# Kernel tuning notes

Measured on AMD Instinct MI355X. Metric: run time of the kernel, lower is better.

The kernel has to match this reference:

```python
import jax, jax.numpy as jnp
import numpy as np

B, S, H = 4, 1024, 1024
NH = 16
DH = H // NH  # 64


def setup_inputs() -> dict:
    key = jax.random.key(0)
    ks = jax.random.split(key, 8)
    std = 1.0 / np.sqrt(H)
    return {
        "query": jax.random.normal(ks[0], (B, S, H), jnp.float32),
        "key": jax.random.normal(ks[1], (B, S, H), jnp.float32),
        "value": jax.random.normal(ks[2], (B, S, H), jnp.float32),
        "masks": jnp.ones((B, S), jnp.float32),
        "Wq": jax.random.normal(ks[3], (H, H), jnp.float32) * std,
        "bq": jnp.zeros((H,), jnp.float32),
        "Wk": jax.random.normal(ks[4], (H, H), jnp.float32) * std,
        "bk": jnp.zeros((H,), jnp.float32),
        "Wv": jax.random.normal(ks[5], (H, H), jnp.float32) * std,
        "bv": jnp.zeros((H,), jnp.float32),
    }


def reference(query, key, value, masks, Wq, bq, Wk, bk, Wv, bv):
    # ReLU-gated projections (torch Linear: x @ W.T + b)
    qp = jax.nn.relu(jnp.einsum("bsh,oh->bso", query, Wq) + bq)
    kp = jax.nn.relu(jnp.einsum("bsh,oh->bso", key, Wk) + bk)
    vp = jax.nn.relu(jnp.einsum("bsh,oh->bso", value, Wv) + bv)
    # chunk(dim=2)+cat(dim=0) == split hidden into (NH, DH) contiguous slices
    qh = qp.reshape(B, S, NH, DH)
    kh = kp.reshape(B, S, NH, DH)
    vh = vp.reshape(B, S, NH, DH)
    scale = 1.0 / jnp.sqrt(jnp.asarray(DH, qp.dtype))
    # [B, NH, Sq, Sk]
    alpha = jnp.einsum("bqnd,bknd->bnqk", qh, kh) * scale
    alpha = jax.nn.softmax(alpha, axis=-1)
    # post-softmax multiplicative mask, applied per QUERY position
    alpha = alpha * masks[:, None, :, None]
    hiddens = jnp.einsum("bnqk,bknd->bqnd", alpha, vh).reshape(B, S, H)
    return hiddens + query
```

## Files before the change

kernel.cpp:

```cpp
#include <hip/hip_runtime.h>


typedef __attribute__((ext_vector_type(8))) __bf16 bf16x8;
typedef __attribute__((ext_vector_type(4))) float f32x4;
typedef __attribute__((ext_vector_type(16))) float f32x16;
typedef __attribute__((ext_vector_type(8))) unsigned short u16x8;
typedef __attribute__((ext_vector_type(4))) unsigned short u16x4;

#define XQ_OFF 0u
#define XK_OFF 4194304u
#define XV_OFF 8388608u
#define WQ_OFF 12582912u
#define WK_OFF 13631488u
#define WV_OFF 14680064u
#define QP_OFF 15728640u
#define KP_OFF 19922944u
#define VT_OFF 24117248u

__device__ __forceinline__ unsigned short f2bf(float f) {
  union { float f; unsigned int u; } c; c.f = f;
  return (unsigned short)((c.u + 0x7fffu + ((c.u >> 16) & 1u)) >> 16);
}

__global__ __launch_bounds__(256) void cvt_kernel(
    const float* __restrict__ q, const float* __restrict__ k, const float* __restrict__ v,
    const float* __restrict__ wq, const float* __restrict__ wk, const float* __restrict__ wv,
    unsigned short* __restrict__ ws) {
  const int z = blockIdx.y;
  const float* src; unsigned short* dst; int n;
  switch (z) {
    case 0: src = q;  dst = ws + XQ_OFF; n = 4194304; break;
    case 1: src = k;  dst = ws + XK_OFF; n = 4194304; break;
    case 2: src = v;  dst = ws + XV_OFF; n = 4194304; break;
    case 3: src = wq; dst = ws + WQ_OFF; n = 1048576; break;
    case 4: src = wk; dst = ws + WK_OFF; n = 1048576; break;
    default: src = wv; dst = ws + WV_OFF; n = 1048576; break;
  }
  const int i8 = (blockIdx.x * 256 + threadIdx.x) * 8;
  if (i8 >= n) return;
  const float4 f0 = *(const float4*)(src + i8);
  const float4 f1 = *(const float4*)(src + i8 + 4);
  u16x8 r;
  r[0] = f2bf(f0.x); r[1] = f2bf(f0.y); r[2] = f2bf(f0.z); r[3] = f2bf(f0.w);
  r[4] = f2bf(f1.x); r[5] = f2bf(f1.y); r[6] = f2bf(f1.z); r[7] = f2bf(f1.w);
  *(u16x8*)(dst + i8) = r;
}

__global__ __launch_bounds__(256) void proj_gemm(
    unsigned short* __restrict__ ws,
    const float* __restrict__ bq, const float* __restrict__ bk, const float* __restrict__ bv) {
  __shared__ unsigned short smem[24576];
  const int z = blockIdx.z;
  const unsigned short* X = ws + (z == 0 ? XQ_OFF : z == 1 ? XK_OFF : XV_OFF);
  const unsigned short* W = ws + (z == 0 ? WQ_OFF : z == 1 ? WK_OFF : WV_OFF);
  unsigned short* P = ws + (z == 0 ? QP_OFF : z == 1 ? KP_OFF : VT_OFF);
  const float* bias = z == 0 ? bq : z == 1 ? bk : bv;

  const int tid  = threadIdx.x;
  const int lane = tid & 63;
  const int w    = tid >> 6;
  const int l31  = lane & 31;
  const int g    = lane >> 5;
  const int wr = w >> 1, wc = w & 1;

  const int lin = blockIdx.x + 8 * blockIdx.y;
  const int xcd = lin & 7;
  const int idx = lin >> 3;
  const int m0 = (xcd * 4 + (idx >> 3)) * 128;
  const int n0 = (idx & 7) * 128;

  f32x16 acc[2][2];
#pragma unroll
  for (int i = 0; i < 2; ++i)
#pragma unroll
    for (int j = 0; j < 2; ++j)
#pragma unroll
      for (int r = 0; r < 16; ++r) acc[i][j][r] = 0.f;

  const int c1 = 256 + tid;
  const int row0 = tid >> 2, kc0 = (((tid & 3) ^ ((row0 >> 1) & 3)) * 8);
  const int row1 = c1 >> 2,  kc1 = (((c1 & 3) ^ ((row1 >> 1) & 3)) * 8);
  const unsigned short* gA0 = X + (size_t)(m0 + row0) * 1024 + kc0;
  const unsigned short* gA1 = X + (size_t)(m0 + row1) * 1024 + kc1;
  const unsigned short* gB0 = W + (size_t)(n0 + row0) * 1024 + kc0;
  const unsigned short* gB1 = W + (size_t)(n0 + row1) * 1024 + kc1;
  const int d0 = w * 512, d1 = 2048 + w * 512;

  auto stage = [&](int buf) {
    unsigned short* Ab = smem + buf * 8192;
    unsigned short* Bb = Ab + 4096;
    __builtin_amdgcn_global_load_lds((const __attribute__((address_space(1))) void*)gA0,
                                     (__attribute__((address_space(3))) void*)(Ab + d0), 16, 0, 0);
    __builtin_amdgcn_global_load_lds((const __attribute__((address_space(1))) void*)gB0,
                                     (__attribute__((address_space(3))) void*)(Bb + d0), 16, 0, 0);
    __builtin_amdgcn_global_load_lds((const __attribute__((address_space(1))) void*)gA1,
                                     (__attribute__((address_space(3))) void*)(Ab + d1), 16, 0, 0);
    __builtin_amdgcn_global_load_lds((const __attribute__((address_space(1))) void*)gB1,
                                     (__attribute__((address_space(3))) void*)(Bb + d1), 16, 0, 0);
    gA0 += 32; gA1 += 32; gB0 += 32; gB1 += 32;
  };
  auto compute = [&](int buf) {
    const unsigned short* Ab = smem + buf * 8192;
    const unsigned short* Bb = Ab + 4096;
    bf16x8 af[2][2], bfv[2][2];
#pragma unroll
    for (int mt = 0; mt < 2; ++mt)
#pragma unroll
      for (int kk = 0; kk < 2; ++kk) {
        const int ra = wr * 64 + mt * 32 + l31;
        af[mt][kk] = *(const bf16x8*)&Ab[ra * 32 + (((kk * 2 + g) ^ ((ra >> 1) & 3)) * 8)];
      }
#pragma unroll
    for (int nt = 0; nt < 2; ++nt)
#pragma unroll
      for (int kk = 0; kk < 2; ++kk) {
        const int rb = wc * 64 + nt * 32 + l31;
        bfv[nt][kk] = *(const bf16x8*)&Bb[rb * 32 + (((kk * 2 + g) ^ ((rb >> 1) & 3)) * 8)];
      }
#pragma unroll
    for (int mt = 0; mt < 2; ++mt)
#pragma unroll
      for (int nt = 0; nt < 2; ++nt)
#pragma unroll
        for (int kk = 0; kk < 2; ++kk)
          acc[mt][nt] = __builtin_amdgcn_mfma_f32_32x32x16_bf16(af[mt][kk], bfv[nt][kk],
                                                                acc[mt][nt], 0, 0, 0);
  };

  stage(0); stage(1);
  for (int t = 0; t < 31; ++t) {
    asm volatile("s_waitcnt vmcnt(4)" ::: "memory");
    __builtin_amdgcn_s_barrier();
    if (t < 30) stage((t + 2) % 3);
    compute(t % 3);
  }
  asm volatile("s_waitcnt vmcnt(0)" ::: "memory");
  __builtin_amdgcn_s_barrier();
  compute(31 % 3);

  asm volatile("s_waitcnt lgkmcnt(0)" ::: "memory");
  __builtin_amdgcn_s_barrier();

  unsigned short* Tw = smem + w * 4608;
  if (z != 2) {
#pragma unroll
    for (int mt = 0; mt < 2; ++mt)
#pragma unroll
      for (int nt = 0; nt < 2; ++nt) {
        const float bvv = bias[n0 + wc * 64 + nt * 32 + l31];
#pragma unroll
        for (int reg = 0; reg < 16; ++reg) {
          const int rloc = (reg & 3) + 8 * (reg >> 2) + 4 * g;
          float v = acc[mt][nt][reg] + bvv;
          v = v > 0.f ? v : 0.f;
          Tw[(mt * 32 + rloc) * 72 + nt * 32 + l31] = f2bf(v);
        }
      }
    const int row0g = m0 + wr * 64;
    const int colb  = n0 + wc * 64;
#pragma unroll
    for (int i = 0; i < 8; ++i) {
      const int rr = i * 8 + (lane >> 3);
      const int cc = (lane & 7) * 8;
      *(u16x8*)&P[(size_t)(row0g + rr) * 1024 + colb + cc] = *(const u16x8*)&Tw[rr * 72 + cc];
    }
  } else {
#pragma unroll
    for (int mt = 0; mt < 2; ++mt)
#pragma unroll
      for (int nt = 0; nt < 2; ++nt) {
        const float bvv = bias[n0 + wc * 64 + nt * 32 + l31];
#pragma unroll
        for (int rq = 0; rq < 4; ++rq) {
          u16x4 pk;
#pragma unroll
          for (int r = 0; r < 4; ++r) {
            float v = acc[mt][nt][rq * 4 + r] + bvv;
            v = v > 0.f ? v : 0.f;
            pk[r] = f2bf(v);
          }
          *(u16x4*)&Tw[(nt * 32 + l31) * 72 + mt * 32 + rq * 8 + g * 4] = pk;
        }
      }
    const int h2 = (n0 >> 6) + wc;
    const int bb = m0 >> 10;
    const int s0 = (m0 & 1023) + wr * 64;
#pragma unroll
    for (int i = 0; i < 8; ++i) {
      const int rr = i * 8 + (lane >> 3);
      const int cc = (lane & 7) * 8;
      *(u16x8*)&P[((size_t)(bb * 16 + h2) * 64 + rr) * 1024 + s0 + cc] =
          *(const u16x8*)&Tw[rr * 72 + cc];
    }
  }
}

__global__ __launch_bounds__(256, 2) void attn_kernel(
    const unsigned short* __restrict__ QP, const unsigned short* __restrict__ KP,
    const unsigned short* __restrict__ VT, const float* __restrict__ masks,
    const float* __restrict__ query, float* __restrict__ out) {
  __shared__ unsigned short Kt[3][64 * 64];
  __shared__ unsigned short Vt[3][64 * 64];
  __shared__ unsigned short Pl[4][32 * 72];
  const int tid  = threadIdx.x;
  const int lane = tid & 63;
  const int w    = tid >> 6;
  const int quad = lane >> 4;
  const int l15  = lane & 15;
  const int bh = blockIdx.x;
  const int b = bh >> 4, h = bh & 15;
  const int q0w = blockIdx.y * 128 + w * 32;
  const size_t base = (size_t)b * 1024 * 1024;

  bf16x8 qf[2][2];
#pragma unroll
  for (int mt = 0; mt < 2; ++mt)
#pragma unroll
    for (int kk = 0; kk < 2; ++kk)
      qf[mt][kk] = *(const bf16x8*)&QP[base + (size_t)(q0w + mt * 16 + l15) * 1024 +
                                       h * 64 + kk * 32 + quad * 8];

  f32x4 o[2][4];
  f32x4 lacc[2];
#pragma unroll
  for (int mt = 0; mt < 2; ++mt) {
    lacc[mt] = f32x4{0.f, 0.f, 0.f, 0.f};
#pragma unroll
    for (int nd = 0; nd < 4; ++nd) o[mt][nd] = f32x4{0.f, 0.f, 0.f, 0.f};
  }

  bf16x8 onesb;
#pragma unroll
  for (int i = 0; i < 8; ++i) onesb[i] = (__bf16)1.0f;

  const int r_st = lane >> 3;
  const int pc   = lane & 7;
  const int swz  = l15 & 7;
  const float cvt = 0.18033688011112042f;

  auto stage = [&](int key0, int buf) {
#pragma unroll
    for (int t = 0; t < 2; ++t) {
      const int rowk = (w * 2 + t) * 8 + r_st;
      const int lc   = pc ^ (rowk & 7);
      const unsigned short* gk = &KP[base + (size_t)(key0 + rowk) * 1024 + h * 64 + lc * 8];
      const unsigned short* gv = &VT[((size_t)bh * 64 + rowk) * 1024 + key0 + lc * 8];
      __builtin_amdgcn_global_load_lds((const __attribute__((address_space(1))) void*)gk,
                                       (__attribute__((address_space(3))) void*)&Kt[buf][(w * 2 + t) * 512],
                                       16, 0, 0);
      __builtin_amdgcn_global_load_lds((const __attribute__((address_space(1))) void*)gv,
                                       (__attribute__((address_space(3))) void*)&Vt[buf][(w * 2 + t) * 512],
                                       16, 0, 0);
    }
  };

  auto step = [&](int buf) {
    const unsigned short* Ktb = Kt[buf];
    const unsigned short* Vtb = Vt[buf];

    bf16x8 kf[2][4];
#pragma unroll
    for (int kk = 0; kk < 2; ++kk)
#pragma unroll
      for (int ni = 0; ni < 4; ++ni)
        kf[kk][ni] = *(const bf16x8*)&Ktb[(ni * 16 + l15) * 64 + ((kk * 4 + quad) ^ swz) * 8];

#pragma unroll
    for (int mt = 0; mt < 2; ++mt) {
      f32x4 st[4];
#pragma unroll
      for (int ni = 0; ni < 4; ++ni) st[ni] = f32x4{0.f, 0.f, 0.f, 0.f};
      __builtin_amdgcn_s_setprio(1);
#pragma unroll
      for (int kk = 0; kk < 2; ++kk)
#pragma unroll
        for (int ni = 0; ni < 4; ++ni)
          st[ni] = __builtin_amdgcn_mfma_f32_16x16x32_bf16(kf[kk][ni], qf[mt][kk], st[ni], 0, 0, 0);
      __builtin_amdgcn_s_setprio(0);
#pragma unroll
      for (int ni = 0; ni < 4; ++ni) {
        float p0 = __builtin_amdgcn_exp2f(fmaf(st[ni][0], cvt, -8.0f));
        float p1 = __builtin_amdgcn_exp2f(fmaf(st[ni][1], cvt, -8.0f));
        float p2 = __builtin_amdgcn_exp2f(fmaf(st[ni][2], cvt, -8.0f));
        float p3 = __builtin_amdgcn_exp2f(fmaf(st[ni][3], cvt, -8.0f));
        const unsigned int u0 = __float_as_uint(p0) + 0x8000u;
        const unsigned int u1 = __float_as_uint(p1) + 0x8000u;
        const unsigned int u2 = __float_as_uint(p2) + 0x8000u;
        const unsigned int u3 = __float_as_uint(p3) + 0x8000u;
        uint2 pk;
        pk.x = (u0 >> 16) | (u1 & 0xffff0000u);
        pk.y = (u2 >> 16) | (u3 & 0xffff0000u);
        *(uint2*)&Pl[w][(mt * 16 + l15) * 72 + ni * 16 + quad * 4] = pk;
      }
    }

#pragma unroll
    for (int kk = 0; kk < 2; ++kk) {
      bf16x8 pa[2];
#pragma unroll
      for (int mt = 0; mt < 2; ++mt)
        pa[mt] = *(const bf16x8*)&Pl[w][(mt * 16 + l15) * 72 + kk * 32 + quad * 8];
      __builtin_amdgcn_s_setprio(1);
#pragma unroll
      for (int mt = 0; mt < 2; ++mt)
        lacc[mt] = __builtin_amdgcn_mfma_f32_16x16x32_bf16(pa[mt], onesb, lacc[mt], 0, 0, 0);
#pragma unroll
      for (int nd = 0; nd < 4; ++nd) {
        bf16x8 vf = *(const bf16x8*)&Vtb[(nd * 16 + l15) * 64 + ((kk * 4 + quad) ^ swz) * 8];
#pragma unroll
        for (int mt = 0; mt < 2; ++mt)
          o[mt][nd] = __builtin_amdgcn_mfma_f32_16x16x32_bf16(pa[mt], vf, o[mt][nd], 0, 0, 0);
      }
      __builtin_amdgcn_s_setprio(0);
    }
  };

  stage(0, 0);
  stage(64, 1);
  for (int kb = 0; kb < 15; ++kb) {
    asm volatile("s_waitcnt vmcnt(4)" ::: "memory");
    __builtin_amdgcn_s_barrier();
    if (kb < 14) stage((kb + 2) * 64, (kb + 2) % 3);
    step(kb % 3);
  }
  asm volatile("s_waitcnt vmcnt(0)" ::: "memory");
  __builtin_amdgcn_s_barrier();
  step(0);

#pragma unroll
  for (int mt = 0; mt < 2; ++mt)
#pragma unroll
    for (int r = 0; r < 4; ++r) {
      const int rq = quad * 4 + r;
      const int row = q0w + mt * 16 + rq;
      const float scale = masks[b * 1024 + row] / lacc[mt][r];
#pragma unroll
      for (int nd = 0; nd < 4; ++nd) {
        const int col = h * 64 + nd * 16 + l15;
        const size_t gi = base + (size_t)row * 1024 + col;
        out[gi] = o[mt][nd][r] * scale + query[gi];
      }
    }
}

extern "C" void kernel_launch(void* const* d_in, const int* in_sizes, int n_in,
                              void* d_out, int out_size, void* d_ws, size_t ws_size,
                              hipStream_t stream) {
  const float* q     = (const float*)d_in[0];
  const float* k     = (const float*)d_in[1];
  const float* v     = (const float*)d_in[2];
  const float* masks = (const float*)d_in[3];
  const float* Wq    = (const float*)d_in[4];
  const float* bq    = (const float*)d_in[5];
  const float* Wk    = (const float*)d_in[6];
  const float* bk    = (const float*)d_in[7];
  const float* Wv    = (const float*)d_in[8];
  const float* bv    = (const float*)d_in[9];
  float* out = (float*)d_out;
  unsigned short* ws = (unsigned short*)d_ws;

  cvt_kernel<<<dim3(2048, 6), 256, 0, stream>>>(q, k, v, Wq, Wk, Wv, ws);
  proj_gemm<<<dim3(8, 32, 3), 256, 0, stream>>>(ws, bq, bk, bv);
  attn_kernel<<<dim3(64, 8), 256, 0, stream>>>(ws + QP_OFF, ws + KP_OFF, ws + VT_OFF,
                                               masks, q, out);
}
```

Before: 172.3 us.

## Fuse fp32-to-bf16 activation conversion into projection GEMM loads

Activations q/k/v are no longer converted to bf16 in a separate pass. The projection GEMM now streams fp32 tiles into LDS with a swizzled layout and converts them to bf16 in registers just before the MFMA. This drops a full read-and-write pass over the three large activation tensors. In exchange, the A-tile loads double in bytes, LDS per stage grows, and the pipeline goes from triple to double buffering with a full vmcnt(0) wait each iteration, which reduces load/compute overlap.

```diff
diff --git a/kernel.cpp b/kernel.cpp
--- a/kernel.cpp
+++ b/kernel.cpp
@@ -7,9 +7,6 @@
 typedef __attribute__((ext_vector_type(8))) unsigned short u16x8;
 typedef __attribute__((ext_vector_type(4))) unsigned short u16x4;
 
-#define XQ_OFF 0u
-#define XK_OFF 4194304u
-#define XV_OFF 8388608u
 #define WQ_OFF 12582912u
 #define WK_OFF 13631488u
 #define WV_OFF 14680064u
@@ -22,22 +19,13 @@
   return (unsigned short)((c.u + 0x7fffu + ((c.u >> 16) & 1u)) >> 16);
 }
 
-__global__ __launch_bounds__(256) void cvt_kernel(
-    const float* __restrict__ q, const float* __restrict__ k, const float* __restrict__ v,
+__global__ __launch_bounds__(256) void cvtw_kernel(
     const float* __restrict__ wq, const float* __restrict__ wk, const float* __restrict__ wv,
     unsigned short* __restrict__ ws) {
   const int z = blockIdx.y;
-  const float* src; unsigned short* dst; int n;
-  switch (z) {
-    case 0: src = q;  dst = ws + XQ_OFF; n = 4194304; break;
-    case 1: src = k;  dst = ws + XK_OFF; n = 4194304; break;
-    case 2: src = v;  dst = ws + XV_OFF; n = 4194304; break;
-    case 3: src = wq; dst = ws + WQ_OFF; n = 1048576; break;
-    case 4: src = wk; dst = ws + WK_OFF; n = 1048576; break;
-    default: src = wv; dst = ws + WV_OFF; n = 1048576; break;
-  }
+  const float* src = z == 0 ? wq : z == 1 ? wk : wv;
+  unsigned short* dst = ws + (z == 0 ? WQ_OFF : z == 1 ? WK_OFF : WV_OFF);
   const int i8 = (blockIdx.x * 256 + threadIdx.x) * 8;
-  if (i8 >= n) return;
   const float4 f0 = *(const float4*)(src + i8);
   const float4 f1 = *(const float4*)(src + i8 + 4);
   u16x8 r;
@@ -47,11 +35,12 @@
 }
 
 __global__ __launch_bounds__(256) void proj_gemm(
+    const float* __restrict__ xq, const float* __restrict__ xk, const float* __restrict__ xv,
     unsigned short* __restrict__ ws,
     const float* __restrict__ bq, const float* __restrict__ bk, const float* __restrict__ bv) {
   __shared__ unsigned short smem[24576];
   const int z = blockIdx.z;
-  const unsigned short* X = ws + (z == 0 ? XQ_OFF : z == 1 ? XK_OFF : XV_OFF);
+  const float* XF = z == 0 ? xq : z == 1 ? xk : xv;
   const unsigned short* W = ws + (z == 0 ? WQ_OFF : z == 1 ? WK_OFF : WV_OFF);
   unsigned short* P = ws + (z == 0 ? QP_OFF : z == 1 ? KP_OFF : VT_OFF);
   const float* bias = z == 0 ? bq : z == 1 ? bk : bv;
@@ -77,38 +66,48 @@
 #pragma unroll
       for (int r = 0; r < 16; ++r) acc[i][j][r] = 0.f;
 
+  const int arow = tid >> 3;
+  const int asrc = (tid & 7) ^ (arow & 7);
+  const float* gAf = XF + (size_t)(m0 + arow) * 1024 + asrc * 4;
   const int c1 = 256 + tid;
-  const int row0 = tid >> 2, kc0 = (((tid & 3) ^ ((row0 >> 1) & 3)) * 8);
-  const int row1 = c1 >> 2,  kc1 = (((c1 & 3) ^ ((row1 >> 1) & 3)) * 8);
-  const unsigned short* gA0 = X + (size_t)(m0 + row0) * 1024 + kc0;
-  const unsigned short* gA1 = X + (size_t)(m0 + row1) * 1024 + kc1;
-  const unsigned short* gB0 = W + (size_t)(n0 + row0) * 1024 + kc0;
-  const unsigned short* gB1 = W + (size_t)(n0 + row1) * 1024 + kc1;
+  const int rowb0 = tid >> 2, kcb0 = (((tid & 3) ^ ((rowb0 >> 1) & 3)) * 8);
+  const int rowb1 = c1 >> 2,  kcb1 = (((c1 & 3) ^ ((rowb1 >> 1) & 3)) * 8);
+  const unsigned short* gB0 = W + (size_t)(n0 + rowb0) * 1024 + kcb0;
+  const unsigned short* gB1 = W + (size_t)(n0 + rowb1) * 1024 + kcb1;
   const int d0 = w * 512, d1 = 2048 + w * 512;
 
   auto stage = [&](int buf) {
-    unsigned short* Ab = smem + buf * 8192;
-    unsigned short* Bb = Ab + 4096;
-    __builtin_amdgcn_global_load_lds((const __attribute__((address_space(1))) void*)gA0,
-                                     (__attribute__((address_space(3))) void*)(Ab + d0), 16, 0, 0);
+    unsigned short* Ab = smem + buf * 12288;
+    unsigned short* Bb = Ab + 8192;
+#pragma unroll
+    for (int j = 0; j < 4; ++j)
+      __builtin_amdgcn_global_load_lds(
+          (const __attribute__((address_space(1))) void*)(gAf + (size_t)j * 32 * 1024),
+          (__attribute__((address_space(3))) void*)(Ab + j * 2048 + w * 512), 16, 0, 0);
     __builtin_amdgcn_global_load_lds((const __attribute__((address_space(1))) void*)gB0,
                                      (__attribute__((address_space(3))) void*)(Bb + d0), 16, 0, 0);
-    __builtin_amdgcn_global_load_lds((const __attribute__((address_space(1))) void*)gA1,
-                                     (__attribute__((address_space(3))) void*)(Ab + d1), 16, 0, 0);
     __builtin_amdgcn_global_load_lds((const __attribute__((address_space(1))) void*)gB1,
                                      (__attribute__((address_space(3))) void*)(Bb + d1), 16, 0, 0);
-    gA0 += 32; gA1 += 32; gB0 += 32; gB1 += 32;
+    gAf += 32; gB0 += 32; gB1 += 32;
   };
+
   auto compute = [&](int buf) {
-    const unsigned short* Ab = smem + buf * 8192;
-    const unsigned short* Bb = Ab + 4096;
+    const float* Af = (const float*)(smem + buf * 12288);
+    const unsigned short* Bb = smem + buf * 12288 + 8192;
     bf16x8 af[2][2], bfv[2][2];
 #pragma unroll
     for (int mt = 0; mt < 2; ++mt)
 #pragma unroll
       for (int kk = 0; kk < 2; ++kk) {
         const int ra = wr * 64 + mt * 32 + l31;
-        af[mt][kk] = *(const bf16x8*)&Ab[ra * 32 + (((kk * 2 + g) ^ ((ra >> 1) & 3)) * 8)];
+        const int s = ra & 7;
+        const int c0 = (kk * 2 + g) * 2;
+        const f32x4 lo = *(const f32x4*)(Af + ra * 32 + ((c0 ^ s) * 4));
+        const f32x4 hi = *(const f32x4*)(Af + ra * 32 + (((c0 + 1) ^ s) * 4));
+        bf16x8 a;
+        a[0] = (__bf16)lo[0]; a[1] = (__bf16)lo[1]; a[2] = (__bf16)lo[2]; a[3] = (__bf16)lo[3];
+        a[4] = (__bf16)hi[0]; a[5] = (__bf16)hi[1]; a[6] = (__bf16)hi[2]; a[7] = (__bf16)hi[3];
+        af[mt][kk] = a;
       }
 #pragma unroll
     for (int nt = 0; nt < 2; ++nt)
@@ -127,16 +126,13 @@
                                                                 acc[mt][nt], 0, 0, 0);
   };
 
-  stage(0); stage(1);
-  for (int t = 0; t < 31; ++t) {
-    asm volatile("s_waitcnt vmcnt(4)" ::: "memory");
+  stage(0);
+  for (int t = 0; t < 32; ++t) {
+    asm volatile("s_waitcnt vmcnt(0)" ::: "memory");
     __builtin_amdgcn_s_barrier();
-    if (t < 30) stage((t + 2) % 3);
-    compute(t % 3);
+    if (t < 31) stage((t + 1) & 1);
+    compute(t & 1);
   }
-  asm volatile("s_waitcnt vmcnt(0)" ::: "memory");
-  __builtin_amdgcn_s_barrier();
-  compute(31 % 3);
 
   asm volatile("s_waitcnt lgkmcnt(0)" ::: "memory");
   __builtin_amdgcn_s_barrier();
@@ -359,8 +355,8 @@
   float* out = (float*)d_out;
   unsigned short* ws = (unsigned short*)d_ws;
 
-  cvt_kernel<<<dim3(2048, 6), 256, 0, stream>>>(q, k, v, Wq, Wk, Wv, ws);
-  proj_gemm<<<dim3(8, 32, 3), 256, 0, stream>>>(ws, bq, bk, bv);
+  cvtw_kernel<<<dim3(512, 3), 256, 0, stream>>>(Wq, Wk, Wv, ws);
+  proj_gemm<<<dim3(8, 32, 3), 256, 0, stream>>>(q, k, v, ws, bq, bk, bv);
   attn_kernel<<<dim3(64, 8), 256, 0, stream>>>(ws + QP_OFF, ws + KP_OFF, ws + VT_OFF,
                                                masks, q, out);
 }
```

After: 204.9 us. 18.9% more time.

## Halve attention query tile per wave and double-buffer K/V for higher occupancy

Applied to the files above, without the earlier changes.

The attention kernel now processes 16 query rows per wave (64 per block) instead of 32, doubling the grid to 64x16 blocks. K/V staging drops from triple to double buffering, and the P scratch shrinks to an XOR-swizzled 16x64 layout with no padding. Launch bounds rise to 4 blocks per SM. The goal is more resident waves to hide latency, traded against halved K/V reuse per LDS load, twice the total K/V traffic, and a full vmcnt(0) wait each iteration that removes prefetch depth.

```diff
diff --git a/kernel.cpp b/kernel.cpp
--- a/kernel.cpp
+++ b/kernel.cpp
@@ -195,13 +195,13 @@
   }
 }
 
-__global__ __launch_bounds__(256, 2) void attn_kernel(
+__global__ __launch_bounds__(256, 4) void attn_kernel(
     const unsigned short* __restrict__ QP, const unsigned short* __restrict__ KP,
     const unsigned short* __restrict__ VT, const float* __restrict__ masks,
     const float* __restrict__ query, float* __restrict__ out) {
-  __shared__ unsigned short Kt[3][64 * 64];
-  __shared__ unsigned short Vt[3][64 * 64];
-  __shared__ unsigned short Pl[4][32 * 72];
+  __shared__ unsigned short Kt[2][64 * 64];
+  __shared__ unsigned short Vt[2][64 * 64];
+  __shared__ unsigned short Pl[4][16 * 64];
   const int tid  = threadIdx.x;
   const int lane = tid & 63;
   const int w    = tid >> 6;
@@ -209,25 +209,19 @@
   const int l15  = lane & 15;
   const int bh = blockIdx.x;
   const int b = bh >> 4, h = bh & 15;
-  const int q0w = blockIdx.y * 128 + w * 32;
+  const int q0w = blockIdx.y * 64 + w * 16;
   const size_t base = (size_t)b * 1024 * 1024;
 
-  bf16x8 qf[2][2];
-#pragma unroll
-  for (int mt = 0; mt < 2; ++mt)
-#pragma unroll
-    for (int kk = 0; kk < 2; ++kk)
-      qf[mt][kk] = *(const bf16x8*)&QP[base + (size_t)(q0w + mt * 16 + l15) * 1024 +
-                                       h * 64 + kk * 32 + quad * 8];
-
-  f32x4 o[2][4];
-  f32x4 lacc[2];
-#pragma unroll
-  for (int mt = 0; mt < 2; ++mt) {
-    lacc[mt] = f32x4{0.f, 0.f, 0.f, 0.f};
-#pragma unroll
-    for (int nd = 0; nd < 4; ++nd) o[mt][nd] = f32x4{0.f, 0.f, 0.f, 0.f};
-  }
+  bf16x8 qf[2];
+#pragma unroll
+  for (int kk = 0; kk < 2; ++kk)
+    qf[kk] = *(const bf16x8*)&QP[base + (size_t)(q0w + l15) * 1024 +
+                                 h * 64 + kk * 32 + quad * 8];
+
+  f32x4 o[4];
+  f32x4 lacc = f32x4{0.f, 0.f, 0.f, 0.f};
+#pragma unroll
+  for (int nd = 0; nd < 4; ++nd) o[nd] = f32x4{0.f, 0.f, 0.f, 0.f};
 
   bf16x8 onesb;
 #pragma unroll
@@ -236,6 +230,7 @@
   const int r_st = lane >> 3;
   const int pc   = lane & 7;
   const int swz  = l15 & 7;
+  const int swzp = (l15 & 7) << 3;
   const float cvt = 0.18033688011112042f;
 
   auto stage = [&](int key0, int buf) {
@@ -265,82 +260,66 @@
       for (int ni = 0; ni < 4; ++ni)
         kf[kk][ni] = *(const bf16x8*)&Ktb[(ni * 16 + l15) * 64 + ((kk * 4 + quad) ^ swz) * 8];
 
-#pragma unroll
-    for (int mt = 0; mt < 2; ++mt) {
-      f32x4 st[4];
-#pragma unroll
-      for (int ni = 0; ni < 4; ++ni) st[ni] = f32x4{0.f, 0.f, 0.f, 0.f};
+    f32x4 st[4];
+#pragma unroll
+    for (int ni = 0; ni < 4; ++ni) st[ni] = f32x4{0.f, 0.f, 0.f, 0.f};
+    __builtin_amdgcn_s_setprio(1);
+#pragma unroll
+    for (int kk = 0; kk < 2; ++kk)
+#pragma unroll
+      for (int ni = 0; ni < 4; ++ni)
+        st[ni] = __builtin_amdgcn_mfma_f32_16x16x32_bf16(kf[kk][ni], qf[kk], st[ni], 0, 0, 0);
+    __builtin_amdgcn_s_setprio(0);
+#pragma unroll
+    for (int ni = 0; ni < 4; ++ni) {
+      float p0 = __builtin_amdgcn_exp2f(fmaf(st[ni][0], cvt, -8.0f));
+      float p1 = __builtin_amdgcn_exp2f(fmaf(st[ni][1], cvt, -8.0f));
+      float p2 = __builtin_amdgcn_exp2f(fmaf(st[ni][2], cvt, -8.0f));
+      float p3 = __builtin_amdgcn_exp2f(fmaf(st[ni][3], cvt, -8.0f));
+      const unsigned int u0 = __float_as_uint(p0) + 0x8000u;
+      const unsigned int u1 = __float_as_uint(p1) + 0x8000u;
+      const unsigned int u2 = __float_as_uint(p2) + 0x8000u;
+      const unsigned int u3 = __float_as_uint(p3) + 0x8000u;
+      uint2 pk;
+      pk.x = (u0 >> 16) | (u1 & 0xffff0000u);
+      pk.y = (u2 >> 16) | (u3 & 0xffff0000u);
+      *(uint2*)&Pl[w][l15 * 64 + ((ni * 16 + quad * 4) ^ swzp)] = pk;
+    }
+
+#pragma unroll
+    for (int kk = 0; kk < 2; ++kk) {
+      bf16x8 pa = *(const bf16x8*)&Pl[w][l15 * 64 + ((kk * 32 + quad * 8) ^ swzp)];
       __builtin_amdgcn_s_setprio(1);
-#pragma unroll
-      for (int kk = 0; kk < 2; ++kk)
-#pragma unroll
-        for (int ni = 0; ni < 4; ++ni)
-          st[ni] = __builtin_amdgcn_mfma_f32_16x16x32_bf16(kf[kk][ni], qf[mt][kk], st[ni], 0, 0, 0);
-      __builtin_amdgcn_s_setprio(0);
-#pragma unroll
-      for (int ni = 0; ni < 4; ++ni) {
-        float p0 = __builtin_amdgcn_exp2f(fmaf(st[ni][0], cvt, -8.0f));
-        float p1 = __builtin_amdgcn_exp2f(fmaf(st[ni][1], cvt, -8.0f));
-        float p2 = __builtin_amdgcn_exp2f(fmaf(st[ni][2], cvt, -8.0f));
-        float p3 = __builtin_amdgcn_exp2f(fmaf(st[ni][3], cvt, -8.0f));
-        const unsigned int u0 = __float_as_uint(p0) + 0x8000u;
-        const unsigned int u1 = __float_as_uint(p1) + 0x8000u;
-        const unsigned int u2 = __float_as_uint(p2) + 0x8000u;
-        const unsigned int u3 = __float_as_uint(p3) + 0x8000u;
-        uint2 pk;
-        pk.x = (u0 >> 16) | (u1 & 0xffff0000u);
-        pk.y = (u2 >> 16) | (u3 & 0xffff0000u);
-        *(uint2*)&Pl[w][(mt * 16 + l15) * 72 + ni * 16 + quad * 4] = pk;
-      }
-    }
-
-#pragma unroll
-    for (int kk = 0; kk < 2; ++kk) {
-      bf16x8 pa[2];
-#pragma unroll
-      for (int mt = 0; mt < 2; ++mt)
-        pa[mt] = *(const bf16x8*)&Pl[w][(mt * 16 + l15) * 72 + kk * 32 + quad * 8];
-      __builtin_amdgcn_s_setprio(1);
-#pragma unroll
-      for (int mt = 0; mt < 2; ++mt)
-        lacc[mt] = __builtin_amdgcn_mfma_f32_16x16x32_bf16(pa[mt], onesb, lacc[mt], 0, 0, 0);
+      lacc = __builtin_amdgcn_mfma_f32_16x16x32_bf16(pa, onesb, lacc, 0, 0, 0);
 #pragma unroll
       for (int nd = 0; nd < 4; ++nd) {
         bf16x8 vf = *(const bf16x8*)&Vtb[(nd * 16 + l15) * 64 + ((kk * 4 + quad) ^ swz) * 8];
-#pragma unroll
-        for (int mt = 0; mt < 2; ++mt)
-          o[mt][nd] = __builtin_amdgcn_mfma_f32_16x16x32_bf16(pa[mt], vf, o[mt][nd], 0, 0, 0);
+        o[nd] = __builtin_amdgcn_mfma_f32_16x16x32_bf16(pa, vf, o[nd], 0, 0, 0);
       }
       __builtin_amdgcn_s_setprio(0);
     }
   };
 
   stage(0, 0);
-  stage(64, 1);
-  for (int kb = 0; kb < 15; ++kb) {
-    asm volatile("s_waitcnt vmcnt(4)" ::: "memory");
+  for (int kb = 0; kb < 16; ++kb) {
+    asm volatile("s_waitcnt vmcnt(0)" ::: "memory");
     __builtin_amdgcn_s_barrier();
-    if (kb < 14) stage((kb + 2) * 64, (kb + 2) % 3);
-    step(kb % 3);
-  }
-  asm volatile("s_waitcnt vmcnt(0)" ::: "memory");
-  __builtin_amdgcn_s_barrier();
-  step(0);
-
-#pragma unroll
-  for (int mt = 0; mt < 2; ++mt)
-#pragma unroll
-    for (int r = 0; r < 4; ++r) {
-      const int rq = quad * 4 + r;
-      const int row = q0w + mt * 16 + rq;
-      const float scale = masks[b * 1024 + row] / lacc[mt][r];
-#pragma unroll
-      for (int nd = 0; nd < 4; ++nd) {
-        const int col = h * 64 + nd * 16 + l15;
-        const size_t gi = base + (size_t)row * 1024 + col;
-        out[gi] = o[mt][nd][r] * scale + query[gi];
-      }
-    }
+    if (kb < 15) stage((kb + 1) * 64, (kb + 1) & 1);
+    step(kb & 1);
+  }
+
+#pragma unroll
+  for (int r = 0; r < 4; ++r) {
+    const int rq = quad * 4 + r;
+    const int row = q0w + rq;
+    const float scale = masks[b * 1024 + row] / lacc[r];
+#pragma unroll
+    for (int nd = 0; nd < 4; ++nd) {
+      const int col = h * 64 + nd * 16 + l15;
+      const size_t gi = base + (size_t)row * 1024 + col;
+      out[gi] = o[nd][r] * scale + query[gi];
+    }
+  }
 }
 
 extern "C" void kernel_launch(void* const* d_in, const int* in_sizes, int n_in,
@@ -361,6 +340,6 @@
 
   cvt_kernel<<<dim3(2048, 6), 256, 0, stream>>>(q, k, v, Wq, Wk, Wv, ws);
   proj_gemm<<<dim3(8, 32, 3), 256, 0, stream>>>(ws, bq, bk, bv);
-  attn_kernel<<<dim3(64, 8), 256, 0, stream>>>(ws + QP_OFF, ws + KP_OFF, ws + VT_OFF,
-                                               masks, q, out);
-}
+  attn_kernel<<<dim3(64, 16), 256, 0, stream>>>(ws + QP_OFF, ws + KP_OFF, ws + VT_OFF,
+                                                masks, q, out);
+}
```

Measured after the change: 173.5 us. No clear change (+0.7%).
